# Optimization experiments

Hardware: AMD Instinct MI355X
Metric: run time of the kernel (lower is better)

The kernel has to match this reference:

```python
import jax, jax.numpy as jnp
from jax import lax
import numpy as np


def _conv(x, w, b, stride=1, pad=1):
    y = lax.conv_general_dilated(x, w, (stride, stride), ((pad, pad), (pad, pad)),
                                 dimension_numbers=('NCHW', 'OIHW', 'NCHW'))
    return y + b[None, :, None, None]


def _deconv(x, w, b):
    # PyTorch ConvTranspose2d(k=3, s=2, p=1, output_padding=1); w is torch layout (Cin, Cout, 3, 3)
    wt = jnp.flip(w, (2, 3)).transpose(1, 0, 2, 3)  # (Cout, Cin, 3, 3)
    y = lax.conv_general_dilated(x, wt, (1, 1), ((1, 2), (1, 2)), lhs_dilation=(2, 2),
                                 dimension_numbers=('NCHW', 'OIHW', 'NCHW'))
    return y + b[None, :, None, None]


def _lrelu(x):
    return jnp.where(x >= 0, x, 0.01 * x)


def _nonlocal(x, tw, tb, pw, pb, gw, gb, ww, wb):
    # embedded-Gaussian non-local block with residual (NONLocalBlock2D)
    B, C, H, W = x.shape
    N = H * W
    th = _conv(x, tw, tb, 1, 0).reshape(B, -1, N)
    ph = _conv(x, pw, pb, 1, 0).reshape(B, -1, N)
    g = _conv(x, gw, gb, 1, 0).reshape(B, -1, N)
    attn = jax.nn.softmax(jnp.einsum('bcn,bcm->bnm', th, ph), axis=-1)  # [B,N,N]
    y = jnp.einsum('bnm,bcm->bcn', attn, g).reshape(B, -1, H, W)
    return _conv(y, ww, wb, 1, 0) + x


def _deform_conv(x, offset, mask, w, b):
    # modulated deformable conv (DCNv2-style), k=3 s=1 p=1, zero padding outside bounds
    B, C, H, W = x.shape
    K2 = 9
    ky, kx = jnp.meshgrid(jnp.arange(3) - 1, jnp.arange(3) - 1, indexing='ij')
    ky = ky.reshape(-1).astype(x.dtype)
    kx = kx.reshape(-1).astype(x.dtype)
    off = offset.reshape(B, K2, 2, H, W)  # (dy, dx) interleaved per kernel tap
    py = jnp.arange(H, dtype=x.dtype)[None, None, :, None] + ky[None, :, None, None] + off[:, :, 0]
    px = jnp.arange(W, dtype=x.dtype)[None, None, None, :] + kx[None, :, None, None] + off[:, :, 1]
    y0 = jnp.floor(py)
    x0 = jnp.floor(px)
    wy1 = py - y0
    wx1 = px - x0
    xf = x.reshape(B, C, H * W)

    def gather(yi, xi):
        valid = ((yi >= 0) & (yi < H) & (xi >= 0) & (xi < W)).astype(x.dtype)
        yc = jnp.clip(yi, 0, H - 1).astype(jnp.int32)
        xc = jnp.clip(xi, 0, W - 1).astype(jnp.int32)
        idx = (yc * W + xc).reshape(B, 1, K2 * H * W)
        v = jnp.take_along_axis(xf, idx, axis=2).reshape(B, C, K2, H, W)
        return v * valid[:, None]

    val = (gather(y0, x0) * ((1 - wy1) * (1 - wx1))[:, None]
           + gather(y0, x0 + 1) * ((1 - wy1) * wx1)[:, None]
           + gather(y0 + 1, x0) * (wy1 * (1 - wx1))[:, None]
           + gather(y0 + 1, x0 + 1) * (wy1 * wx1)[:, None])
    val = val * mask[:, None]  # modulation
    return jnp.einsum('bckhw,ock->bohw', val, w.reshape(w.shape[0], C, K2)) + b[None, :, None, None]


def _forward(x_all, ms_fine, ms_coarse, enc_w0, enc_b0, enc_w1, enc_b1,
             nl0_tw, nl0_tb, nl0_pw, nl0_pb, nl0_gw, nl0_gb, nl0_ww, nl0_wb,
             nl1_tw, nl1_tb, nl1_pw, nl1_pb, nl1_gw, nl1_gb, nl1_ww, nl1_wb,
             dec_w0, dec_b0, dec_w1, dec_b1, off_w, off_b, dcn_w, dcn_b):
    def motion(pc, cc, pf, cf):
        # scale 0 (coarse, reversed order), mot_mode='concat'
        e0 = _lrelu(_conv(jnp.concatenate([pc, cc], 1), enc_w0, enc_b0, 2, 1))
        m0 = e0 + _nonlocal(e0, nl0_tw, nl0_tb, nl0_pw, nl0_pb, nl0_gw, nl0_gb, nl0_ww, nl0_wb)
        u0 = _lrelu(_deconv(m0, dec_w0, dec_b0))
        # scale 1 (fine)
        e1 = _lrelu(_conv(jnp.concatenate([pf, cf], 1), enc_w1, enc_b1, 2, 1))
        m1 = e1 + _nonlocal(e1, nl1_tw, nl1_tb, nl1_pw, nl1_pb, nl1_gw, nl1_gb, nl1_ww, nl1_wb)
        return _lrelu(_deconv(m1 + u0, dec_w1, dec_b1))

    aligned = [x_all[0]]
    for s in range(1, x_all.shape[0]):  # seq_len - 1 alignments
        mot = motion(ms_coarse[s], ms_coarse[0], ms_fine[s], ms_fine[0])
        est = _conv(mot, off_w, off_b, 1, 1)  # [B, 27, H, W]
        offset = est[:, 9:]
        mask = jax.nn.sigmoid(est[:, :9])
        aligned.append(_deform_conv(x_all[s], offset, mask, dcn_w, dcn_b))
    return jnp.stack(aligned)


def setup_inputs() -> dict:
    key = jax.random.key(0)
    ks = iter(jax.random.split(key, 48))

    def rn(shape, scale=1.0):
        return jax.random.normal(next(ks), shape, dtype=jnp.float32) * scale

    S, B = 3, 2
    inp = {
        'x_all': rn((S, B, 128, 128, 128)),
        'ms_fine': rn((S, B, 128, 128, 128)),
        'ms_coarse': rn((S, B, 256, 64, 64)),
        'enc_w0': rn((64, 512, 3, 3), 0.02), 'enc_b0': rn((64,), 0.02),
        'enc_w1': rn((64, 256, 3, 3), 0.02), 'enc_b1': rn((64,), 0.02),
    }
    for i in range(2):
        inp[f'nl{i}_tw'] = rn((32, 64, 1, 1), 0.05); inp[f'nl{i}_tb'] = rn((32,), 0.02)
        inp[f'nl{i}_pw'] = rn((32, 64, 1, 1), 0.05); inp[f'nl{i}_pb'] = rn((32,), 0.02)
        inp[f'nl{i}_gw'] = rn((32, 64, 1, 1), 0.05); inp[f'nl{i}_gb'] = rn((32,), 0.02)
        inp[f'nl{i}_ww'] = rn((64, 32, 1, 1), 0.05); inp[f'nl{i}_wb'] = rn((64,), 0.02)
    inp['dec_w0'] = rn((64, 64, 3, 3), 0.05); inp['dec_b0'] = rn((64,), 0.02)
    inp['dec_w1'] = rn((64, 64, 3, 3), 0.05); inp['dec_b1'] = rn((64,), 0.02)
    inp['off_w'] = rn((27, 64, 3, 3), 0.02); inp['off_b'] = rn((27,), 0.02)
    inp['dcn_w'] = rn((128, 128, 3, 3), 0.03); inp['dcn_b'] = rn((128,), 0.02)
    return inp


def reference(x_all, ms_fine, ms_coarse, enc_w0, enc_b0, enc_w1, enc_b1,
              nl0_tw, nl0_tb, nl0_pw, nl0_pb, nl0_gw, nl0_gb, nl0_ww, nl0_wb,
              nl1_tw, nl1_tb, nl1_pw, nl1_pb, nl1_gw, nl1_gb, nl1_ww, nl1_wb,
              dec_w0, dec_b0, dec_w1, dec_b1, off_w, off_b, dcn_w, dcn_b):
    return _forward(x_all, ms_fine, ms_coarse, enc_w0, enc_b0, enc_w1, enc_b1,
                    nl0_tw, nl0_tb, nl0_pw, nl0_pb, nl0_gw, nl0_gb, nl0_ww, nl0_wb,
                    nl1_tw, nl1_tb, nl1_pw, nl1_pb, nl1_gw, nl1_gb, nl1_ww, nl1_wb,
                    dec_w0, dec_b0, dec_w1, dec_b1, off_w, off_b, dcn_w, dcn_b)
```

## Files before the change

### kernel.cpp

```cpp
#include <hip/hip_runtime.h>
#include <math.h>

typedef __attribute__((ext_vector_type(8))) short bf16x8;
typedef __attribute__((ext_vector_type(4))) float f32x4;
typedef unsigned short ushort_t;
typedef unsigned int uint_t;

__device__ __forceinline__ float lrelu_f(float x) { return x >= 0.f ? x : 0.01f * x; }

__device__ __forceinline__ ushort_t f2bf(float f) {
    uint_t x = __float_as_uint(f);
    uint_t r = (x + 0x7fffu + ((x >> 16) & 1u)) >> 16;
    return (ushort_t)r;
}

__device__ __forceinline__ uint_t pack_bf16(float lo, float hi) {
    uint_t out;
    asm("v_cvt_pk_bf16_f32 %0, %1, %2" : "=v"(out) : "v"(lo), "v"(hi));
    return out;
}

__global__ __launch_bounds__(256) void castw2_kernel(const float* __restrict__ w,
    ushort_t* __restrict__ w2, int Cout, int Cin, int K, int deconv)
{
    int idx = blockIdx.x * 256 + threadIdx.x;
    if (idx >= 64 * K) return;
    int co = idx / K, kp = idx % K;
    int cb = kp / 288;
    int r  = kp % 288;
    int tap = r >> 5, cl = r & 31;
    int ci = cb * 32 + cl;
    float val = 0.f;
    if (co < Cout)
        val = deconv ? w[(size_t)(ci * Cout + co) * 9 + (8 - tap)]
                     : w[(size_t)(co * Cin + ci) * 9 + tap];
    w2[idx] = f2bf(val);
}

template<int STRIDE, int MODE>
__global__ __launch_bounds__(256) void conv3x3_mfma(
    const float* __restrict__ inA, const float* __restrict__ inB, int CinA,
    size_t sStrideA, int Hin, int Win, int Cin,
    const ushort_t* __restrict__ w2, int K,
    int Wout, int Npx, int tilesPerMap, int ksplit, int chunksPerKs,
    float* __restrict__ part,
    const float* __restrict__ bias, int act, int CoutStore, float* __restrict__ outDirect)
{
    __shared__ ushort_t sB[64 * 40];
    int tile = blockIdx.x % tilesPerMap;
    int ks   = (blockIdx.x / tilesPerMap) % ksplit;
    int b4   = blockIdx.x / (tilesPerMap * ksplit);
    int s_idx = b4 >> 1, bb = b4 & 1;
    int tid  = threadIdx.x;
    int wave = tid >> 6, lane = tid & 63;
    int lrow = lane & 15, lkg = lane >> 4;
    int px  = tid & 63;
    int cio = wave * 8;
    int p   = tile * 64 + px;
    int oy  = p / Wout, ox = p - oy * Wout;
    int HWin = Hin * Win;
    int CinB = Cin - CinA;

    f32x4 acc[4];
    #pragma unroll
    for (int n2 = 0; n2 < 4; ++n2) acc[n2] = (f32x4){0.f, 0.f, 0.f, 0.f};

    for (int cch = 0; cch < chunksPerKs; ++cch) {
        int chunkIdx = ks * chunksPerKs + cch;
        int cb  = chunkIdx / 9;
        int tap = chunkIdx - cb * 9;
        int cib = cb * 32;
        int ky = tap / 3, kx = tap - ky * 3;
        float msk;
        int offp;
        if (MODE == 0) {
            int iy = oy * STRIDE - 1 + ky;
            int ix = ox * STRIDE - 1 + kx;
            bool vld = (iy >= 0) && (iy < Hin) && (ix >= 0) && (ix < Win);
            msk = vld ? 1.f : 0.f;
            offp = min(max(iy, 0), Hin - 1) * Win + min(max(ix, 0), Win - 1);
        } else {
            int uy = oy + ky, ux = ox + kx;
            int r = (uy - 1) >> 1, q = (ux - 1) >> 1;
            bool vld = (uy & 1) && (ux & 1) && (r < Hin) && (q < Win);
            msk = vld ? 1.f : 0.f;
            offp = min(max(r, 0), Hin - 1) * Win + min(max(q, 0), Win - 1);
        }
        int c = cib + cio;
        const float* src = (c < CinA)
            ? inA + s_idx * sStrideA + (size_t)(bb * CinA + c) * HWin
            : inB + (size_t)(bb * CinB + (c - CinA)) * HWin;
        float v[8];
        #pragma unroll
        for (int j = 0; j < 8; ++j) v[j] = src[(size_t)j * HWin + offp] * msk;
        uint4 pk;
        pk.x = pack_bf16(v[0], v[1]);
        pk.y = pack_bf16(v[2], v[3]);
        pk.z = pack_bf16(v[4], v[5]);
        pk.w = pack_bf16(v[6], v[7]);
        __syncthreads();
        *(uint4*)&sB[px * 40 + cio] = pk;
        __syncthreads();

        const ushort_t* wr = w2 + (size_t)(wave * 16 + lrow) * K + chunkIdx * 32 + lkg * 8;
        bf16x8 afr = *(const bf16x8*)wr;
        #pragma unroll
        for (int n2 = 0; n2 < 4; ++n2) {
            bf16x8 bfr = *(const bf16x8*)&sB[(n2 * 16 + lrow) * 40 + lkg * 8];
            acc[n2] = __builtin_amdgcn_mfma_f32_16x16x32_bf16(afr, bfr, acc[n2], 0, 0, 0);
        }
    }

    if (bias) {
        #pragma unroll
        for (int n2 = 0; n2 < 4; ++n2) {
            #pragma unroll
            for (int j = 0; j < 4; ++j) {
                int co = wave * 16 + lkg * 4 + j;
                if (co < CoutStore) {
                    int pp = tile * 64 + n2 * 16 + lrow;
                    float r = acc[n2][j] + bias[co];
                    if (act) r = lrelu_f(r);
                    outDirect[((size_t)(b4 * CoutStore + co)) * (size_t)Npx + pp] = r;
                }
            }
        }
    } else {
        #pragma unroll
        for (int n2 = 0; n2 < 4; ++n2) {
            #pragma unroll
            for (int j = 0; j < 4; ++j) {
                int co = wave * 16 + lkg * 4 + j;
                int pp = tile * 64 + n2 * 16 + lrow;
                part[((size_t)(ks * 4 + b4) * 64 + co) * (size_t)Npx + pp] = acc[n2][j];
            }
        }
    }
}

__global__ __launch_bounds__(256) void reduce_bias_act(const float* __restrict__ part,
    const float* __restrict__ bias, float* __restrict__ out,
    int Cout, int Npx, int ksplit, int act)
{
    int idx = blockIdx.x * 256 + threadIdx.x;
    int total = 4 * Cout * Npx;
    if (idx >= total) return;
    int p  = idx % Npx;
    int co = (idx / Npx) % Cout;
    int b4 = idx / (Npx * Cout);
    float s = bias[co];
    for (int ks = 0; ks < ksplit; ++ks)
        s += part[(((size_t)ks * 4 + b4) * 64 + co) * (size_t)Npx + p];
    if (act) s = lrelu_f(s);
    out[((size_t)b4 * Cout + co) * (size_t)Npx + p] = s;
}

__global__ __launch_bounds__(256) void castw_perm_kernel(const float* __restrict__ w,
    ushort_t* __restrict__ wbf)
{
    int idx = blockIdx.x * 256 + threadIdx.x;
    if (idx >= 147456) return;
    int co = idx / 1152;
    int r  = idx % 1152;
    int chunk = r / 288;
    int r2 = r % 288;
    int tap = r2 >> 5;
    int cl  = r2 & 31;
    int ci = chunk * 32 + cl;
    wbf[idx] = f2bf(w[(size_t)co * 1152 + ci * 9 + tap]);
}

__global__ __launch_bounds__(256) void transpose_nhwc_kernel(const float* __restrict__ x,
    float* __restrict__ xT)
{
    __shared__ float t[32][33];
    int cT = blockIdx.x & 3;
    int pT = (blockIdx.x >> 2) & 511;
    int b  = blockIdx.x >> 11;
    int tx = threadIdx.x & 31, ty = threadIdx.x >> 5;
    const float* src = x + ((size_t)b * 128 + cT * 32) * 16384 + (size_t)pT * 32;
    #pragma unroll
    for (int i = 0; i < 4; ++i)
        t[ty + 8 * i][tx] = src[(size_t)(ty + 8 * i) * 16384 + tx];
    __syncthreads();
    float* dst = xT + ((size_t)b * 16384 + (size_t)pT * 32) * 128 + cT * 32;
    #pragma unroll
    for (int i = 0; i < 4; ++i)
        dst[(size_t)(ty + 8 * i) * 128 + tx] = t[tx][ty + 8 * i];
}

__global__ __launch_bounds__(256) void conv1x1x3_bf16(const float* __restrict__ e, int N,
    const float* __restrict__ tw, const float* __restrict__ tb,
    const float* __restrict__ pw, const float* __restrict__ pb,
    const float* __restrict__ gw, const float* __restrict__ gb,
    ushort_t* __restrict__ thT, ushort_t* __restrict__ phT, ushort_t* __restrict__ gT)
{
    __shared__ float sw[32 * 64];
    __shared__ float sb[32];
    int tid = threadIdx.x;
    int idx = blockIdx.x * 256 + tid;
    int j = idx / (4 * N);
    const float* wsel = (j == 0) ? tw : (j == 1) ? pw : gw;
    const float* bsel = (j == 0) ? tb : (j == 1) ? pb : gb;
    for (int i = tid; i < 2048; i += 256) sw[i] = wsel[i];
    if (tid < 32) sb[tid] = bsel[tid];
    __syncthreads();
    int rem = idx - j * 4 * N;
    int n = rem % N, b4 = rem / N;
    float ein[64];
    const float* ep = e + (size_t)b4 * 64 * N + n;
    #pragma unroll
    for (int ci = 0; ci < 64; ++ci) ein[ci] = ep[(size_t)ci * N];

    float val[32];
    #pragma unroll
    for (int cc = 0; cc < 32; ++cc) {
        float acc = sb[cc];
        const float* wr = &sw[cc * 64];
        #pragma unroll
        for (int ci = 0; ci < 64; ++ci) acc = fmaf(wr[ci], ein[ci], acc);
        val[cc] = acc;
    }
    if (j < 2) {
        ushort_t* row = (j == 0 ? thT : phT) + ((size_t)b4 * N + n) * 32;
        #pragma unroll
        for (int w4 = 0; w4 < 4; ++w4) {
            uint4 pk;
            pk.x = pack_bf16(val[8 * w4 + 0], val[8 * w4 + 1]);
            pk.y = pack_bf16(val[8 * w4 + 2], val[8 * w4 + 3]);
            pk.z = pack_bf16(val[8 * w4 + 4], val[8 * w4 + 5]);
            pk.w = pack_bf16(val[8 * w4 + 6], val[8 * w4 + 7]);
            *(uint4*)(row + 8 * w4) = pk;
        }
    } else {
        #pragma unroll
        for (int cc = 0; cc < 32; ++cc)
            gT[((size_t)b4 * 32 + cc) * N + n] = f2bf(val[cc]);
    }
}

__global__ __launch_bounds__(256) void attn_flash(const ushort_t* __restrict__ thT,
    const ushort_t* __restrict__ phT, const ushort_t* __restrict__ gT,
    float* __restrict__ partO, float* __restrict__ partML, int N, int KVS)
{
    __shared__ ushort_t sP[4][16 * 40];
    int tid  = threadIdx.x;
    int wave = tid >> 6, lane = tid & 63;
    int lq = lane & 15, lkg = lane >> 4;
    int nqb = N / 64;
    int ks = blockIdx.x % KVS;
    int qb = (blockIdx.x / KVS) % nqb;
    int b4 = blockIdx.x / (KVS * nqb);
    int q0w = qb * 64 + wave * 16;
    int chunk = N / KVS;
    int m_start = ks * chunk;

    bf16x8 qf = *(const bf16x8*)(thT + ((size_t)b4 * N + q0w + lq) * 32 + 8 * lkg);

    float m_run = -1e30f, l_run = 0.f;
    f32x4 acc[2];
    acc[0] = (f32x4){0.f, 0.f, 0.f, 0.f};
    acc[1] = (f32x4){0.f, 0.f, 0.f, 0.f};

    for (int m0 = m_start; m0 < m_start + chunk; m0 += 64) {
        f32x4 tf[4];
        #pragma unroll
        for (int f = 0; f < 4; ++f) {
            bf16x8 kf = *(const bf16x8*)(phT + ((size_t)b4 * N + m0 + f * 16 + lq) * 32 + 8 * lkg);
            tf[f] = __builtin_amdgcn_mfma_f32_16x16x32_bf16(kf, qf,
                        (f32x4){0.f, 0.f, 0.f, 0.f}, 0, 0, 0);
        }

        float mx = -1e30f;
        #pragma unroll
        for (int f = 0; f < 4; ++f)
            #pragma unroll
            for (int r = 0; r < 4; ++r) mx = fmaxf(mx, tf[f][r]);
        mx = fmaxf(mx, __shfl_xor(mx, 16));
        mx = fmaxf(mx, __shfl_xor(mx, 32));
        float m_new = fmaxf(m_run, mx);
        float scale = __expf(m_run - m_new);
        float rs = 0.f;
        #pragma unroll
        for (int f = 0; f < 4; ++f)
            #pragma unroll
            for (int r = 0; r < 4; ++r) {
                float pv = __expf(tf[f][r] - m_new);
                tf[f][r] = pv;
                rs += pv;
            }
        rs += __shfl_xor(rs, 16);
        rs += __shfl_xor(rs, 32);
        l_run = l_run * scale + rs;
        m_run = m_new;

        float sc[4];
        #pragma unroll
        for (int r = 0; r < 4; ++r) sc[r] = __shfl(scale, 4 * lkg + r);
        #pragma unroll
        for (int h = 0; h < 2; ++h)
            #pragma unroll
            for (int r = 0; r < 4; ++r) acc[h][r] *= sc[r];

        #pragma unroll
        for (int f = 0; f < 4; ++f) {
            *(uint_t*)&sP[wave][lq * 40 + f * 16 + 4 * lkg]     = pack_bf16(tf[f][0], tf[f][1]);
            *(uint_t*)&sP[wave][lq * 40 + f * 16 + 4 * lkg + 2] = pack_bf16(tf[f][2], tf[f][3]);
        }

        #pragma unroll
        for (int mc = 0; mc < 2; ++mc) {
            bf16x8 pf = *(const bf16x8*)&sP[wave][lq * 40 + mc * 32 + 8 * lkg];
            #pragma unroll
            for (int h = 0; h < 2; ++h) {
                bf16x8 vf = *(const bf16x8*)(gT + ((size_t)b4 * 32 + h * 16 + lq) * N
                                             + m0 + mc * 32 + 8 * lkg);
                acc[h] = __builtin_amdgcn_mfma_f32_16x16x32_bf16(pf, vf, acc[h], 0, 0, 0);
            }
        }
    }

    #pragma unroll
    for (int h = 0; h < 2; ++h) {
        #pragma unroll
        for (int r = 0; r < 4; ++r) {
            int q = q0w + 4 * lkg + r;
            partO[(((size_t)ks * 4 + b4) * N + q) * 32 + h * 16 + lq] = acc[h][r];
        }
    }
    if (lane < 16) {
        size_t mlo = (((size_t)ks * 4 + b4) * N + q0w + lq) * 2;
        partML[mlo]     = m_run;
        partML[mlo + 1] = l_run;
    }
}

__global__ __launch_bounds__(256) void nl_merge_fused(const float* __restrict__ e,
    const float* __restrict__ partO, const float* __restrict__ partML,
    const float* __restrict__ u,
    const float* __restrict__ ww, const float* __restrict__ wb,
    float* __restrict__ out, int N, int KVS)
{
    __shared__ float sw[64 * 32];
    __shared__ float sb[64];
    int tid = threadIdx.x;
    for (int i = tid; i < 2048; i += 256) sw[i] = ww[i];
    if (tid < 64) sb[tid] = wb[tid];
    __syncthreads();
    int idx = blockIdx.x * 256 + tid;
    int n = idx % N;
    int cog = (idx / N) & 3;
    int b4 = idx / (4 * N);

    float mstar = -1e30f;
    for (int ks = 0; ks < KVS; ++ks)
        mstar = fmaxf(mstar, partML[(((size_t)ks * 4 + b4) * N + n) * 2]);
    float denom = 0.f;
    float yv[32];
    #pragma unroll
    for (int c = 0; c < 32; ++c) yv[c] = 0.f;
    for (int ks = 0; ks < KVS; ++ks) {
        size_t mlo = (((size_t)ks * 4 + b4) * N + n) * 2;
        float w = __expf(partML[mlo] - mstar);
        denom += w * partML[mlo + 1];
        const f32x4* op = (const f32x4*)(partO + (((size_t)ks * 4 + b4) * N + n) * 32);
        #pragma unroll
        for (int jj = 0; jj < 8; ++jj) {
            f32x4 v = op[jj];
            #pragma unroll
            for (int t = 0; t < 4; ++t) yv[4 * jj + t] = fmaf(w, v[t], yv[4 * jj + t]);
        }
    }
    float inv = 1.f / denom;
    #pragma unroll
    for (int i = 0; i < 16; ++i) {
        int co = cog * 16 + i;
        float dot = 0.f;
        const float* wr = &sw[co * 32];
        #pragma unroll
        for (int c = 0; c < 32; ++c) dot = fmaf(wr[c], yv[c], dot);
        size_t o = (size_t)b4 * 64 * N + (size_t)co * N + n;
        float r = sb[co] + inv * dot + 2.f * e[o];
        if (u) r += u[o];
        out[o] = r;
    }
}

__global__ __launch_bounds__(256) void deform_mfma3(const float* __restrict__ xT,
    const float* __restrict__ est, const ushort_t* __restrict__ wbf,
    const float* __restrict__ bias, float* __restrict__ out)
{
    const int H = 128, W = 128, HW = 16384;
    const int BS = 296;
    __shared__ ushort_t sB[64 * BS];
    __shared__ float4 sW[576];
    __shared__ uint2  sO[576];
    int id  = blockIdx.x;
    int lin = (id & 7) * 64 + (id >> 3);
    int tile = lin & 255;
    int b    = lin >> 8;
    int p0   = tile * 64;
    int tid  = threadIdx.x;

    const float* eb = est + (size_t)b * 27 * HW;
    for (int i = tid; i < 576; i += 256) {
        int k = i >> 6, j = i & 63;
        int p = p0 + j;
        int yy = p >> 7, xx = p & 127;
        float oy = eb[(size_t)(9 + 2 * k) * HW + p];
        float ox = eb[(size_t)(10 + 2 * k) * HW + p];
        float mv = eb[(size_t)k * HW + p];
        float mk = 1.f / (1.f + __expf(-mv));
        float py = (float)(yy + (k / 3) - 1) + oy;
        float qx = (float)(xx + (k % 3) - 1) + ox;
        float fy0 = floorf(py), fx0 = floorf(qx);
        float wy = py - fy0, wx = qx - fx0;
        int y0 = (int)fy0, x0 = (int)fx0;
        int y1 = y0 + 1, x1 = x0 + 1;
        bool yv0 = (y0 >= 0) && (y0 < H), yv1 = (y1 >= 0) && (y1 < H);
        bool xv0 = (x0 >= 0) && (x0 < W), xv1 = (x1 >= 0) && (x1 < W);
        int y0c = min(max(y0, 0), H - 1), y1c = min(max(y1, 0), H - 1);
        int x0c = min(max(x0, 0), W - 1), x1c = min(max(x1, 0), W - 1);
        float4 w4;
        w4.x = (yv0 && xv0) ? (1.f - wy) * (1.f - wx) * mk : 0.f;
        w4.y = (yv0 && xv1) ? (1.f - wy) * wx * mk : 0.f;
        w4.z = (yv1 && xv0) ? wy * (1.f - wx) * mk : 0.f;
        w4.w = (yv1 && xv1) ? wy * wx * mk : 0.f;
        sW[i] = w4;
        uint_t o00 = (uint_t)(y0c * W + x0c), o01 = (uint_t)(y0c * W + x1c);
        uint_t o10 = (uint_t)(y1c * W + x0c), o11 = (uint_t)(y1c * W + x1c);
        sO[i] = (uint2){ o00 | (o01 << 16), o10 | (o11 << 16) };
    }

    int wave = tid >> 6, lane = tid & 63;
    int co_base = wave * 32;
    int lrow = lane & 15, lkg = lane >> 4;

    f32x4 acc[2][4];
    #pragma unroll
    for (int m2 = 0; m2 < 2; ++m2)
        #pragma unroll
        for (int n2 = 0; n2 < 4; ++n2) acc[m2][n2] = (f32x4){0.f, 0.f, 0.f, 0.f};

    const f32x4* xb4 = (const f32x4*)(xT + (size_t)b * HW * 128);

    for (int cc = 0; cc < 128; cc += 32) {
        __syncthreads();
        #pragma unroll 2
        for (int it = 0; it < 18; ++it) {
            int task = it * 256 + tid;
            int cg = task & 7;
            int si = task >> 3;
            float4 w4 = sW[si];
            uint2 o4 = sO[si];
            int chv = (cc >> 2) + cg;
            f32x4 c00 = xb4[(o4.x & 0xFFFFu) * 32 + chv];
            f32x4 c01 = xb4[(o4.x >> 16) * 32 + chv];
            f32x4 c10 = xb4[(o4.y & 0xFFFFu) * 32 + chv];
            f32x4 c11 = xb4[(o4.y >> 16) * 32 + chv];
            f32x4 v;
            #pragma unroll
            for (int j = 0; j < 4; ++j)
                v[j] = w4.x * c00[j] + w4.y * c01[j] + w4.z * c10[j] + w4.w * c11[j];
            int pxl = si & 63, tap = si >> 6;
            uint2 pk;
            pk.x = pack_bf16(v[0], v[1]);
            pk.y = pack_bf16(v[2], v[3]);
            *(uint2*)&sB[pxl * BS + tap * 32 + cg * 4] = pk;
        }
        __syncthreads();
        int kbase = cc * 9;
        #pragma unroll
        for (int ks = 0; ks < 9; ++ks) {
            bf16x8 afr[2], bfr[4];
            #pragma unroll
            for (int m2 = 0; m2 < 2; ++m2)
                afr[m2] = *reinterpret_cast<const bf16x8*>(
                    wbf + (size_t)(co_base + m2 * 16 + lrow) * 1152 + kbase + ks * 32 + lkg * 8);
            #pragma unroll
            for (int n2 = 0; n2 < 4; ++n2)
                bfr[n2] = *reinterpret_cast<const bf16x8*>(
                    &sB[(n2 * 16 + lrow) * BS + ks * 32 + lkg * 8]);
            #pragma unroll
            for (int m2 = 0; m2 < 2; ++m2)
                #pragma unroll
                for (int n2 = 0; n2 < 4; ++n2)
                    acc[m2][n2] = __builtin_amdgcn_mfma_f32_16x16x32_bf16(
                        afr[m2], bfr[n2], acc[m2][n2], 0, 0, 0);
        }
    }

    #pragma unroll
    for (int m2 = 0; m2 < 2; ++m2) {
        #pragma unroll
        for (int j = 0; j < 4; ++j) {
            int co = co_base + m2 * 16 + lkg * 4 + j;
            float bb = bias[co];
            #pragma unroll
            for (int n2 = 0; n2 < 4; ++n2) {
                int px = p0 + n2 * 16 + lrow;
                out[((size_t)(b * 128 + co)) * HW + px] = acc[m2][n2][j] + bb;
            }
        }
    }
}

extern "C" void kernel_launch(void* const* d_in, const int* in_sizes, int n_in,
                              void* d_out, int out_size, void* d_ws, size_t ws_size,
                              hipStream_t stream)
{
    const float* x_all     = (const float*)d_in[0];
    const float* ms_fine   = (const float*)d_in[1];
    const float* ms_coarse = (const float*)d_in[2];
    const float* enc_w0 = (const float*)d_in[3];
    const float* enc_b0 = (const float*)d_in[4];
    const float* enc_w1 = (const float*)d_in[5];
    const float* enc_b1 = (const float*)d_in[6];
    const float* nl_tw[2] = { (const float*)d_in[7],  (const float*)d_in[15] };
    const float* nl_tb[2] = { (const float*)d_in[8],  (const float*)d_in[16] };
    const float* nl_pw[2] = { (const float*)d_in[9],  (const float*)d_in[17] };
    const float* nl_pb[2] = { (const float*)d_in[10], (const float*)d_in[18] };
    const float* nl_gw[2] = { (const float*)d_in[11], (const float*)d_in[19] };
    const float* nl_gb[2] = { (const float*)d_in[12], (const float*)d_in[20] };
    const float* nl_ww[2] = { (const float*)d_in[13], (const float*)d_in[21] };
    const float* nl_wb[2] = { (const float*)d_in[14], (const float*)d_in[22] };
    const float* dec_w0 = (const float*)d_in[23];
    const float* dec_b0 = (const float*)d_in[24];
    const float* dec_w1 = (const float*)d_in[25];
    const float* dec_b1 = (const float*)d_in[26];
    const float* off_w  = (const float*)d_in[27];
    const float* off_b  = (const float*)d_in[28];
    const float* dcn_w  = (const float*)d_in[29];
    const float* dcn_b  = (const float*)d_in[30];

    float* ws = (float*)d_ws;
    ushort_t* wbf     = (ushort_t*)ws;
    ushort_t* w2_enc0 = wbf + 147456;
    ushort_t* w2_enc1 = w2_enc0 + 294912;
    ushort_t* w2_dec0 = w2_enc1 + 147456;
    ushort_t* w2_dec1 = w2_dec0 + 36864;
    ushort_t* w2_est  = w2_dec1 + 36864;
    float* U1      = ws + 350208;
    float* u0      = U1 + 1048576;
    float* e1      = u0 + 1048576;
    float* partML  = e1 + 1048576;
    float* regPart = partML + 163840;
    float* regMot  = regPart + 2097152;

    float* e0 = U1;
    ushort_t* thT0 = (ushort_t*)(U1 + 262144);
    ushort_t* phT0 = thT0 + 131072;
    ushort_t* gT0  = phT0 + 131072;
    float* m0 = U1 + 458752;
    ushort_t* thT1 = (ushort_t*)U1;
    ushort_t* phT1 = thT1 + 524288;
    ushort_t* gT1  = phT1 + 524288;
    float* m1  = U1;
    float* mot = regMot;
    float* xT  = regMot;
    float* est = regPart;

    float* out = (float*)d_out;
    const size_t frame  = (size_t)2 * 128 * 128 * 128;
    const size_t cframe = (size_t)2 * 256 * 64 * 64;

    hipMemcpyAsync(out, x_all, frame * sizeof(float), hipMemcpyDeviceToDevice, stream);

    castw_perm_kernel<<<(147456 + 255) / 256, 256, 0, stream>>>(dcn_w, wbf);
    castw2_kernel<<<(64 * 4608 + 255) / 256, 256, 0, stream>>>(enc_w0, w2_enc0, 64, 512, 4608, 0);
    castw2_kernel<<<(64 * 2304 + 255) / 256, 256, 0, stream>>>(enc_w1, w2_enc1, 64, 256, 2304, 0);
    castw2_kernel<<<(64 * 576 + 255) / 256, 256, 0, stream>>>(dec_w0, w2_dec0, 64, 64, 576, 1);
    castw2_kernel<<<(64 * 576 + 255) / 256, 256, 0, stream>>>(dec_w1, w2_dec1, 64, 64, 576, 1);
    castw2_kernel<<<(64 * 576 + 255) / 256, 256, 0, stream>>>(off_w, w2_est, 27, 64, 576, 0);


    conv3x3_mfma<2, 0><<<4 * 16 * 8, 256, 0, stream>>>(
        ms_coarse + cframe, ms_coarse, 256, cframe, 64, 64, 512,
        w2_enc0, 4608, 32, 1024, 16, 8, 18, regPart, nullptr, 0, 0, nullptr);
    reduce_bias_act<<<1024, 256, 0, stream>>>(regPart, enc_b0, e0, 64, 1024, 8, 1);

    conv1x1x3_bf16<<<48, 256, 0, stream>>>(e0, 1024,
        nl_tw[0], nl_tb[0], nl_pw[0], nl_pb[0], nl_gw[0], nl_gb[0], thT0, phT0, gT0);
    attn_flash<<<4 * 16 * 8, 256, 0, stream>>>(thT0, phT0, gT0, regPart, partML, 1024, 8);
    nl_merge_fused<<<64, 256, 0, stream>>>(e0, regPart, partML, nullptr,
        nl_ww[0], nl_wb[0], m0, 1024, 8);

    conv3x3_mfma<1, 1><<<4 * 64 * 2, 256, 0, stream>>>(
        m0, m0, 64, (size_t)2 * 64 * 1024, 32, 32, 64,
        w2_dec0, 576, 64, 4096, 64, 2, 9, regPart, nullptr, 0, 0, nullptr);
    reduce_bias_act<<<4096, 256, 0, stream>>>(regPart, dec_b0, u0, 64, 4096, 2, 1);

    conv3x3_mfma<2, 0><<<4 * 64 * 2, 256, 0, stream>>>(
        ms_fine + frame, ms_fine, 128, frame, 128, 128, 256,
        w2_enc1, 2304, 64, 4096, 64, 2, 36, regPart, nullptr, 0, 0, nullptr);
    reduce_bias_act<<<4096, 256, 0, stream>>>(regPart, enc_b1, e1, 64, 4096, 2, 1);

    conv1x1x3_bf16<<<192, 256, 0, stream>>>(e1, 4096,
        nl_tw[1], nl_tb[1], nl_pw[1], nl_pb[1], nl_gw[1], nl_gb[1], thT1, phT1, gT1);
    attn_flash<<<4 * 64 * 4, 256, 0, stream>>>(thT1, phT1, gT1, regPart, partML, 4096, 4);
    nl_merge_fused<<<256, 256, 0, stream>>>(e1, regPart, partML, u0,
        nl_ww[1], nl_wb[1], m1, 4096, 4);

    conv3x3_mfma<1, 1><<<4 * 256, 256, 0, stream>>>(
        m1, m1, 64, (size_t)2 * 64 * 4096, 64, 64, 64,
        w2_dec1, 576, 128, 16384, 256, 1, 18, regPart, dec_b1, 1, 64, mot);

    conv3x3_mfma<1, 0><<<4 * 256, 256, 0, stream>>>(
        mot, mot, 64, (size_t)2 * 64 * 16384, 128, 128, 64,
        w2_est, 576, 128, 16384, 256, 1, 18, regPart, off_b, 0, 27, est);

    for (int s = 1; s < 3; ++s) {
        transpose_nhwc_kernel<<<4096, 256, 0, stream>>>(x_all + (size_t)s * frame, xT);
        deform_mfma3<<<512, 256, 0, stream>>>(
            xT, est + (size_t)(s - 1) * 2 * 27 * 16384, wbf, dcn_b,
            out + (size_t)s * frame);
    }
}
```

Before: 378.8 us.

## Use bf16 NHWC input for deform conv, batch frames, exp2 softmax with lazy rescale

```diff
diff --git a/kernel.cpp b/kernel.cpp
--- a/kernel.cpp
+++ b/kernel.cpp
@@ -18,6 +18,12 @@
     uint_t out;
     asm("v_cvt_pk_bf16_f32 %0, %1, %2" : "=v"(out) : "v"(lo), "v"(hi));
     return out;
+}
+
+__device__ __forceinline__ float fexp2(float x) {
+    float r;
+    asm("v_exp_f32 %0, %1" : "=v"(r) : "v"(x));
+    return r;
 }
 
 __global__ __launch_bounds__(256) void castw2_kernel(const float* __restrict__ w,
@@ -170,23 +176,23 @@
     wbf[idx] = f2bf(w[(size_t)co * 1152 + ci * 9 + tap]);
 }
 
-__global__ __launch_bounds__(256) void transpose_nhwc_kernel(const float* __restrict__ x,
-    float* __restrict__ xT)
+__global__ __launch_bounds__(256) void transpose_nhwc_bf16(const float* __restrict__ x,
+    ushort_t* __restrict__ xT)
 {
     __shared__ float t[32][33];
     int cT = blockIdx.x & 3;
     int pT = (blockIdx.x >> 2) & 511;
-    int b  = blockIdx.x >> 11;
+    int b4 = blockIdx.x >> 11;
     int tx = threadIdx.x & 31, ty = threadIdx.x >> 5;
-    const float* src = x + ((size_t)b * 128 + cT * 32) * 16384 + (size_t)pT * 32;
+    const float* src = x + ((size_t)((b4 + 2) * 128) + cT * 32) * 16384 + (size_t)pT * 32;
     #pragma unroll
     for (int i = 0; i < 4; ++i)
         t[ty + 8 * i][tx] = src[(size_t)(ty + 8 * i) * 16384 + tx];
     __syncthreads();
-    float* dst = xT + ((size_t)b * 16384 + (size_t)pT * 32) * 128 + cT * 32;
+    ushort_t* dst = xT + ((size_t)b4 * 16384 + (size_t)pT * 32) * 128 + cT * 32;
     #pragma unroll
     for (int i = 0; i < 4; ++i)
-        dst[(size_t)(ty + 8 * i) * 128 + tx] = t[tx][ty + 8 * i];
+        dst[(size_t)(ty + 8 * i) * 128 + tx] = f2bf(t[tx][ty + 8 * i]);
 }
 
 __global__ __launch_bounds__(256) void conv1x1x3_bf16(const float* __restrict__ e, int N,
@@ -221,6 +227,10 @@
         for (int ci = 0; ci < 64; ++ci) acc = fmaf(wr[ci], ein[ci], acc);
         val[cc] = acc;
     }
+    if (j == 0) {
+        #pragma unroll
+        for (int cc = 0; cc < 32; ++cc) val[cc] *= 1.44269504f;
+    }
     if (j < 2) {
         ushort_t* row = (j == 0 ? thT : phT) + ((size_t)b4 * N + n) * 32;
         #pragma unroll
@@ -278,29 +288,33 @@
             for (int r = 0; r < 4; ++r) mx = fmaxf(mx, tf[f][r]);
         mx = fmaxf(mx, __shfl_xor(mx, 16));
         mx = fmaxf(mx, __shfl_xor(mx, 32));
-        float m_new = fmaxf(m_run, mx);
-        float scale = __expf(m_run - m_new);
+
+        if (__any(mx > m_run)) {
+            float m_new = fmaxf(m_run, mx);
+            float scale = fexp2(m_run - m_new);
+            l_run *= scale;
+            m_run = m_new;
+            float sc[4];
+            #pragma unroll
+            for (int r = 0; r < 4; ++r) sc[r] = __shfl(scale, 4 * lkg + r);
+            #pragma unroll
+            for (int h = 0; h < 2; ++h)
+                #pragma unroll
+                for (int r = 0; r < 4; ++r) acc[h][r] *= sc[r];
+        }
+
         float rs = 0.f;
         #pragma unroll
         for (int f = 0; f < 4; ++f)
             #pragma unroll
             for (int r = 0; r < 4; ++r) {
-                float pv = __expf(tf[f][r] - m_new);
+                float pv = fexp2(tf[f][r] - m_run);
                 tf[f][r] = pv;
                 rs += pv;
             }
         rs += __shfl_xor(rs, 16);
         rs += __shfl_xor(rs, 32);
-        l_run = l_run * scale + rs;
-        m_run = m_new;
-
-        float sc[4];
-        #pragma unroll
-        for (int r = 0; r < 4; ++r) sc[r] = __shfl(scale, 4 * lkg + r);
-        #pragma unroll
-        for (int h = 0; h < 2; ++h)
-            #pragma unroll
-            for (int r = 0; r < 4; ++r) acc[h][r] *= sc[r];
+        l_run += rs;
 
         #pragma unroll
         for (int f = 0; f < 4; ++f) {
@@ -361,7 +375,7 @@
     for (int c = 0; c < 32; ++c) yv[c] = 0.f;
     for (int ks = 0; ks < KVS; ++ks) {
         size_t mlo = (((size_t)ks * 4 + b4) * N + n) * 2;
-        float w = __expf(partML[mlo] - mstar);
+        float w = fexp2(partML[mlo] - mstar);
         denom += w * partML[mlo + 1];
         const f32x4* op = (const f32x4*)(partO + (((size_t)ks * 4 + b4) * N + n) * 32);
         #pragma unroll
@@ -386,7 +400,7 @@
     }
 }
 
-__global__ __launch_bounds__(256) void deform_mfma3(const float* __restrict__ xT,
+__global__ __launch_bounds__(256) void deform_mfma4(const ushort_t* __restrict__ xT,
     const float* __restrict__ est, const ushort_t* __restrict__ wbf,
     const float* __restrict__ bias, float* __restrict__ out)
 {
@@ -396,13 +410,13 @@
     __shared__ float4 sW[576];
     __shared__ uint2  sO[576];
     int id  = blockIdx.x;
-    int lin = (id & 7) * 64 + (id >> 3);
+    int lin = (id & 7) * 128 + (id >> 3);
     int tile = lin & 255;
-    int b    = lin >> 8;
+    int b4   = lin >> 8;
     int p0   = tile * 64;
     int tid  = threadIdx.x;
 
-    const float* eb = est + (size_t)b * 27 * HW;
+    const float* eb = est + (size_t)b4 * 27 * HW;
     for (int i = tid; i < 576; i += 256) {
         int k = i >> 6, j = i & 63;
         int p = p0 + j;
@@ -442,31 +456,43 @@
         #pragma unroll
         for (int n2 = 0; n2 < 4; ++n2) acc[m2][n2] = (f32x4){0.f, 0.f, 0.f, 0.f};
 
-    const f32x4* xb4 = (const f32x4*)(xT + (size_t)b * HW * 128);
+    const ushort_t* xb = xT + (size_t)b4 * HW * 128;
 
     for (int cc = 0; cc < 128; cc += 32) {
         __syncthreads();
-        #pragma unroll 2
-        for (int it = 0; it < 18; ++it) {
+        #pragma unroll 3
+        for (int it = 0; it < 9; ++it) {
             int task = it * 256 + tid;
-            int cg = task & 7;
-            int si = task >> 3;
+            int cg = task & 3;
+            int si = task >> 2;
             float4 w4 = sW[si];
             uint2 o4 = sO[si];
-            int chv = (cc >> 2) + cg;
-            f32x4 c00 = xb4[(o4.x & 0xFFFFu) * 32 + chv];
-            f32x4 c01 = xb4[(o4.x >> 16) * 32 + chv];
-            f32x4 c10 = xb4[(o4.y & 0xFFFFu) * 32 + chv];
-            f32x4 c11 = xb4[(o4.y >> 16) * 32 + chv];
-            f32x4 v;
-            #pragma unroll
-            for (int j = 0; j < 4; ++j)
-                v[j] = w4.x * c00[j] + w4.y * c01[j] + w4.z * c10[j] + w4.w * c11[j];
+            int chb = cc + cg * 8;
+            uint4 u00 = *(const uint4*)(xb + (size_t)(o4.x & 0xFFFFu) * 128 + chb);
+            uint4 u01 = *(const uint4*)(xb + (size_t)(o4.x >> 16) * 128 + chb);
+            uint4 u10 = *(const uint4*)(xb + (size_t)(o4.y & 0xFFFFu) * 128 + chb);
+            uint4 u11 = *(const uint4*)(xb + (size_t)(o4.y >> 16) * 128 + chb);
+            float v[8];
+            const uint_t* a0 = (const uint_t*)&u00;
+            const uint_t* a1 = (const uint_t*)&u01;
+            const uint_t* a2 = (const uint_t*)&u10;
+            const uint_t* a3 = (const uint_t*)&u11;
+            #pragma unroll
+            for (int q = 0; q < 4; ++q) {
+                float c00l = __uint_as_float(a0[q] << 16), c00h = __uint_as_float(a0[q] & 0xffff0000u);
+                float c01l = __uint_as_float(a1[q] << 16), c01h = __uint_as_float(a1[q] & 0xffff0000u);
+                float c10l = __uint_as_float(a2[q] << 16), c10h = __uint_as_float(a2[q] & 0xffff0000u);
+                float c11l = __uint_as_float(a3[q] << 16), c11h = __uint_as_float(a3[q] & 0xffff0000u);
+                v[2 * q]     = w4.x * c00l + w4.y * c01l + w4.z * c10l + w4.w * c11l;
+                v[2 * q + 1] = w4.x * c00h + w4.y * c01h + w4.z * c10h + w4.w * c11h;
+            }
             int pxl = si & 63, tap = si >> 6;
-            uint2 pk;
+            uint4 pk;
             pk.x = pack_bf16(v[0], v[1]);
             pk.y = pack_bf16(v[2], v[3]);
-            *(uint2*)&sB[pxl * BS + tap * 32 + cg * 4] = pk;
+            pk.z = pack_bf16(v[4], v[5]);
+            pk.w = pack_bf16(v[6], v[7]);
+            *(uint4*)&sB[pxl * BS + tap * 32 + cg * 8] = pk;
         }
         __syncthreads();
         int kbase = cc * 9;
@@ -499,7 +525,7 @@
             #pragma unroll
             for (int n2 = 0; n2 < 4; ++n2) {
                 int px = p0 + n2 * 16 + lrow;
-                out[((size_t)(b * 128 + co)) * HW + px] = acc[m2][n2][j] + bb;
+                out[((size_t)((b4 + 2) * 128 + co)) * HW + px] = acc[m2][n2][j] + bb;
             }
         }
     }
@@ -544,7 +570,7 @@
     float* u0      = U1 + 1048576;
     float* e1      = u0 + 1048576;
     float* partML  = e1 + 1048576;
-    float* regPart = partML + 163840;
+    float* regPart = partML + 262144;
     float* regMot  = regPart + 2097152;
 
     float* e0 = U1;
@@ -557,8 +583,9 @@
     ushort_t* gT1  = phT1 + 524288;
     float* m1  = U1;
     float* mot = regMot;
-    float* xT  = regMot;
+    ushort_t* xTb = (ushort_t*)regMot;
     float* est = regPart;
+    float* partO1 = regMot;
 
     float* out = (float*)d_out;
     const size_t frame  = (size_t)2 * 128 * 128 * 128;
@@ -597,9 +624,9 @@
 
     conv1x1x3_bf16<<<192, 256, 0, stream>>>(e1, 4096,
         nl_tw[1], nl_tb[1], nl_pw[1], nl_pb[1], nl_gw[1], nl_gb[1], thT1, phT1, gT1);
-    attn_flash<<<4 * 64 * 4, 256, 0, stream>>>(thT1, phT1, gT1, regPart, partML, 4096, 4);
-    nl_merge_fused<<<256, 256, 0, stream>>>(e1, regPart, partML, u0,
-        nl_ww[1], nl_wb[1], m1, 4096, 4);
+    attn_flash<<<4 * 64 * 8, 256, 0, stream>>>(thT1, phT1, gT1, partO1, partML, 4096, 8);
+    nl_merge_fused<<<256, 256, 0, stream>>>(e1, partO1, partML, u0,
+        nl_ww[1], nl_wb[1], m1, 4096, 8);
 
     conv3x3_mfma<1, 1><<<4 * 256, 256, 0, stream>>>(
         m1, m1, 64, (size_t)2 * 64 * 4096, 64, 64, 64,
@@ -609,10 +636,6 @@
         mot, mot, 64, (size_t)2 * 64 * 16384, 128, 128, 64,
         w2_est, 576, 128, 16384, 256, 1, 18, regPart, off_b, 0, 27, est);
 
-    for (int s = 1; s < 3; ++s) {
-        transpose_nhwc_kernel<<<4096, 256, 0, stream>>>(x_all + (size_t)s * frame, xT);
-        deform_mfma3<<<512, 256, 0, stream>>>(
-            xT, est + (size_t)(s - 1) * 2 * 27 * 16384, wbf, dcn_b,
-            out + (size_t)s * frame);
-    }
-}
+    transpose_nhwc_bf16<<<8192, 256, 0, stream>>>(x_all, xTb);
+    deform_mfma4<<<1024, 256, 0, stream>>>(xTb, est, wbf, dcn_b, out);
+}
```

After: 363.6 us. -4.0%, faster.
